# Kernel tuning notes

Hardware: AMD Instinct MI355X
Metric: run time of the kernel (lower is better)

The kernel has to match this reference:

```python
import jax, jax.numpy as jnp
import numpy as np

MARGIN = 0.3
EPS = 1e-6  # torch.nn.functional.pairwise_distance eps


def setup_inputs() -> dict:
    key = jax.random.key(0)
    k1, k2 = jax.random.split(key)
    B, D, C = 8192, 256, 512
    embeddings = jax.random.normal(k1, (B, D), dtype=jnp.float32)
    labels = jax.random.randint(k2, (B,), 0, C, dtype=jnp.int64)
    return {"embeddings": embeddings, "labels": labels}


def reference(embeddings, labels):
    B = embeddings.shape[0]
    # pairwise squared L2 via GEMM
    dot = embeddings @ embeddings.T                      # [B, B]
    sq = jnp.diag(dot)[:, None] + jnp.diag(dot)[None, :] - 2.0 * dot
    dist_sq = jnp.clip(sq, 0.0)

    same = labels[:, None] == labels[None, :]            # [B, B] bool
    eye = jnp.eye(B, dtype=bool)
    pos_mask = same & ~eye
    neg_mask = ~same

    valid = pos_mask.any(axis=1) & neg_mask.any(axis=1)  # [B]
    INF = dist_sq.max() + 1.0

    hardest_pos_idx = jnp.argmax(dist_sq * pos_mask.astype(dist_sq.dtype), axis=1)
    hardest_neg_idx = jnp.argmin(dist_sq + same.astype(dist_sq.dtype) * INF, axis=1)

    a = embeddings
    p = embeddings[hardest_pos_idx]
    n = embeddings[hardest_neg_idx]
    # torch pairwise_distance: ||x1 - x2 + eps||_2
    d_ap = jnp.linalg.norm(a - p + EPS, axis=1)
    d_an = jnp.linalg.norm(a - n + EPS, axis=1)
    per_anchor = jnp.maximum(d_ap - d_an + MARGIN, 0.0)

    v = valid.astype(per_anchor.dtype)
    n_valid = v.sum()
    loss = jnp.where(n_valid > 0, (per_anchor * v).sum() / jnp.maximum(n_valid, 1.0), 0.0)
    return loss
```

## Files before the change

kernel.cpp:

```cpp
#include <hip/hip_runtime.h>
#include <math.h>

#define NB 8192
#define ND 256
#define MARGIN_F 0.3f
#define EPS_F 1e-6f
#define BIAS_F 512.0f
#define NFIN 2048

typedef __attribute__((ext_vector_type(8))) short bf16x8;
typedef __attribute__((ext_vector_type(4))) float f32x4;

__device__ __forceinline__ unsigned short f2bf(float x) {
    unsigned int u = __float_as_uint(x);
    return (unsigned short)((u + 0x7fffu + ((u >> 16) & 1u)) >> 16);
}

__device__ __forceinline__ void gld16(const void* g, void* l) {
    __builtin_amdgcn_global_load_lds(
        (const __attribute__((address_space(1))) void*)g,
        (__attribute__((address_space(3))) void*)l, 16, 0, 0);
}

__global__ __launch_bounds__(512) void prep_k(const float* __restrict__ emb,
                                              unsigned short* __restrict__ ehi,
                                              float* __restrict__ sqnb,
                                              unsigned int* __restrict__ pos_key,
                                              unsigned int* __restrict__ neg_key) {
    const int tid = threadIdx.x;
    const int bid = blockIdx.x;
    const size_t base = (size_t)bid * 4096;

    const float4 v0 = *reinterpret_cast<const float4*>(&emb[base + tid * 8]);
    const float4 v1 = *reinterpret_cast<const float4*>(&emb[base + tid * 8 + 4]);
    ushort4 h0, h1;
    h0.x = f2bf(v0.x); h0.y = f2bf(v0.y); h0.z = f2bf(v0.z); h0.w = f2bf(v0.w);
    h1.x = f2bf(v1.x); h1.y = f2bf(v1.y); h1.z = f2bf(v1.z); h1.w = f2bf(v1.w);

    const int row_l = tid >> 5;
    const int kk = tid & 31;
    const int dst = (kk >> 2) * 512 + ((kk & 3) * 16 + row_l) * 8;
    *reinterpret_cast<ushort4*>(&ehi[base + dst])     = h0;
    *reinterpret_cast<ushort4*>(&ehi[base + dst + 4]) = h1;

    if (tid >= 64 && tid < 80)  pos_key[bid * 16 + (tid - 64)] = 0u;
    if (tid >= 80 && tid < 96)  neg_key[bid * 16 + (tid - 80)] = 0xFFFFFFFFu;

    float s = v0.x * v0.x + v0.y * v0.y + v0.z * v0.z + v0.w * v0.w
            + v1.x * v1.x + v1.y * v1.y + v1.z * v1.z + v1.w * v1.w;
#pragma unroll
    for (int m = 1; m <= 16; m <<= 1) s += __shfl_xor(s, m, 64);
    if (kk == 0) sqnb[bid * 16 + row_l] = s + BIAS_F;
}

template <bool DIAG>
__device__ __forceinline__ void mine_tile(
        const f32x4 (&acc)[2][4], const float (&sqjc)[4], const int (&lblc)[4],
        const unsigned (&enc)[4], const int* __restrict__ lbl_i_s,
        unsigned (&pmax)[8], unsigned (&nmin)[8],
        int i_base, int jb, int wrow, int q, int lx) {
#pragma unroll
    for (int tr = 0; tr < 2; ++tr) {
#pragma unroll
        for (int reg = 0; reg < 4; ++reg) {
            const int r = tr * 4 + reg;
            const int rowb = wrow + tr * 16 + q * 4 + reg;
            const int lab = lbl_i_s[rowb];
            unsigned pk[4], nk[4];
#pragma unroll
            for (int tc = 0; tc < 4; ++tc) {
                const float v = fmaf(-2.0f, acc[tr][tc][reg], sqjc[tc]);
                const unsigned key = (__float_as_uint(v) & 0xFFFFE000u) | enc[tc];
                const bool same = (lblc[tc] == lab);
                bool pc = same;
                if (DIAG) pc = same && ((jb + tc * 16 + lx) != (i_base + rowb));
                pk[tc] = pc ? key : 0u;
                nk[tc] = same ? 0xFFFFFFFFu : key;
            }
            const unsigned pa = pk[0] >= pk[1] ? pk[0] : pk[1];
            const unsigned pb = pk[2] >= pk[3] ? pk[2] : pk[3];
            const unsigned pm = pa >= pb ? pa : pb;
            pmax[r] = pmax[r] >= pm ? pmax[r] : pm;
            const unsigned na = nk[0] <= nk[1] ? nk[0] : nk[1];
            const unsigned nb = nk[2] <= nk[3] ? nk[2] : nk[3];
            const unsigned nm = na <= nb ? na : nb;
            nmin[r] = nmin[r] <= nm ? nmin[r] : nm;
        }
    }
}

__global__ __launch_bounds__(256, 4) void pair_k(
        const unsigned short* __restrict__ ehi, const float* __restrict__ sqnb,
        const int* __restrict__ labels,
        unsigned int* __restrict__ pos_key, unsigned int* __restrict__ neg_key) {
    __shared__ short Bsh[32 * 512];
    __shared__ int   lbl_i_s[128];

    const int tid = threadIdx.x;
    const int w = tid >> 6;
    const int lane = tid & 63;
    const int q = lane >> 4;
    const int lx = lane & 15;
    const int bid = blockIdx.x;
    const int slice = bid & 15;
    const int i_base = (bid >> 4) * 128;
    const int wrow = w * 32;
    const int g0 = (i_base >> 4) + w * 2;

    if (tid < 128) lbl_i_s[tid] = labels[i_base + tid];

    unsigned pmax[8], nmin[8];
#pragma unroll
    for (int r = 0; r < 8; ++r) { pmax[r] = 0u; nmin[r] = 0xFFFFFFFFu; }

#pragma unroll 1
    for (int jt = 0; jt < 8; ++jt) {
        const int jb = slice * 512 + jt * 64;
        __syncthreads();
        {
            const unsigned short* srcB = ehi + (size_t)(jb >> 4) * 4096;
#pragma unroll
            for (int p = 0; p < 8; ++p)
                gld16(srcB + ((size_t)p * 256 + tid) * 8, Bsh + (p * 256 + tid) * 8);
        }
        int lblc[4]; float sqjc[4]; unsigned enc[4];
#pragma unroll
        for (int tc = 0; tc < 4; ++tc) {
            const int jj = jb + tc * 16 + lx;
            lblc[tc] = labels[jj];
            sqjc[tc] = sqnb[jj];
            enc[tc] = 8191u - (unsigned)jj;
        }
        bf16x8 a0[2], a1[2], n0[2], n1[2];
#pragma unroll
        for (int tr = 0; tr < 2; ++tr) {
            a0[tr] = *(const bf16x8*)&ehi[((size_t)(g0 + tr) * 8 + 0) * 512 + lane * 8];
            a1[tr] = *(const bf16x8*)&ehi[((size_t)(g0 + tr) * 8 + 1) * 512 + lane * 8];
        }
        __syncthreads();

        f32x4 acc[2][4];
#pragma unroll
        for (int a = 0; a < 2; ++a)
#pragma unroll
            for (int b = 0; b < 4; ++b) acc[a][b] = (f32x4){0.f, 0.f, 0.f, 0.f};

#pragma unroll 1
        for (int kb2 = 0; kb2 < 4; ++kb2) {
            const int kbe = kb2 * 2, kbo = kbe + 1;
            const int kn0 = (kbe + 2) & 7, kn1 = (kbe + 3) & 7;
#pragma unroll
            for (int tr = 0; tr < 2; ++tr) {
                n0[tr] = *(const bf16x8*)&ehi[((size_t)(g0 + tr) * 8 + kn0) * 512 + lane * 8];
                n1[tr] = *(const bf16x8*)&ehi[((size_t)(g0 + tr) * 8 + kn1) * 512 + lane * 8];
            }
            {
                bf16x8 bh[4];
#pragma unroll
                for (int tc = 0; tc < 4; ++tc)
                    bh[tc] = *(const bf16x8*)&Bsh[(tc * 8 + kbe) * 512 + lane * 8];
#pragma unroll
                for (int tr = 0; tr < 2; ++tr)
#pragma unroll
                    for (int tc = 0; tc < 4; ++tc)
                        acc[tr][tc] = __builtin_amdgcn_mfma_f32_16x16x32_bf16(
                            a0[tr], bh[tc], acc[tr][tc], 0, 0, 0);
            }
            {
                bf16x8 bh[4];
#pragma unroll
                for (int tc = 0; tc < 4; ++tc)
                    bh[tc] = *(const bf16x8*)&Bsh[(tc * 8 + kbo) * 512 + lane * 8];
#pragma unroll
                for (int tr = 0; tr < 2; ++tr)
#pragma unroll
                    for (int tc = 0; tc < 4; ++tc)
                        acc[tr][tc] = __builtin_amdgcn_mfma_f32_16x16x32_bf16(
                            a1[tr], bh[tc], acc[tr][tc], 0, 0, 0);
            }
#pragma unroll
            for (int tr = 0; tr < 2; ++tr) { a0[tr] = n0[tr]; a1[tr] = n1[tr]; }
        }

        if ((unsigned)(jb - i_base) < 128u)
            mine_tile<true>(acc, sqjc, lblc, enc, lbl_i_s, pmax, nmin, i_base, jb, wrow, q, lx);
        else
            mine_tile<false>(acc, sqjc, lblc, enc, lbl_i_s, pmax, nmin, i_base, jb, wrow, q, lx);
    }

#pragma unroll
    for (int r = 0; r < 8; ++r) {
        unsigned pm = pmax[r], nm = nmin[r];
#pragma unroll
        for (int mm = 1; mm < 16; mm <<= 1) {
            const unsigned pm2 = __shfl_xor(pm, mm, 64);
            const unsigned nm2 = __shfl_xor(nm, mm, 64);
            pm = pm >= pm2 ? pm : pm2;
            nm = nm <= nm2 ? nm : nm2;
        }
        if (lx == r) {
            const int row = i_base + wrow + (r >> 2) * 16 + q * 4 + (r & 3);
            atomicMax(&pos_key[row], pm);
            atomicMin(&neg_key[row], nm);
        }
    }
}

__global__ __launch_bounds__(256) void final_k(
        const float* __restrict__ emb,
        const unsigned int* __restrict__ pos_key, const unsigned int* __restrict__ neg_key,
        float* __restrict__ pbsum, float* __restrict__ pbcnt) {
    __shared__ float ssum[4], scnt[4];
    const int w = threadIdx.x >> 6;
    const int lane = threadIdx.x & 63;
    const int i = blockIdx.x * 4 + w;

    const unsigned pk = pos_key[i], nk = neg_key[i];
    const int pi = 8191 - (int)(pk & 8191u);
    const int ni = 8191 - (int)(nk & 8191u);
    const bool valid = (pk != 0u) && (nk != 0xFFFFFFFFu);

    const float4 av  = *reinterpret_cast<const float4*>(&emb[(size_t)i  * ND + lane * 4]);
    const float4 pvv = *reinterpret_cast<const float4*>(&emb[(size_t)pi * ND + lane * 4]);
    const float4 nvv = *reinterpret_cast<const float4*>(&emb[(size_t)ni * ND + lane * 4]);
    float sap, san;
    {
        const float d0 = av.x - pvv.x + EPS_F, d1 = av.y - pvv.y + EPS_F;
        const float d2 = av.z - pvv.z + EPS_F, d3 = av.w - pvv.w + EPS_F;
        sap = d0 * d0 + d1 * d1 + d2 * d2 + d3 * d3;
        const float e0 = av.x - nvv.x + EPS_F, e1 = av.y - nvv.y + EPS_F;
        const float e2 = av.z - nvv.z + EPS_F, e3 = av.w - nvv.w + EPS_F;
        san = e0 * e0 + e1 * e1 + e2 * e2 + e3 * e3;
    }
#pragma unroll
    for (int m = 32; m; m >>= 1) {
        sap += __shfl_down(sap, m, 64);
        san += __shfl_down(san, m, 64);
    }
    if (lane == 0) {
        const float per = fmaxf(sqrtf(sap) - sqrtf(san) + MARGIN_F, 0.0f);
        ssum[w] = valid ? per : 0.0f;
        scnt[w] = valid ? 1.0f : 0.0f;
    }
    __syncthreads();
    if (threadIdx.x == 0) {
        pbsum[blockIdx.x] = ssum[0] + ssum[1] + ssum[2] + ssum[3];
        pbcnt[blockIdx.x] = scnt[0] + scnt[1] + scnt[2] + scnt[3];
    }
}

__global__ __launch_bounds__(256) void reduce_k(const float* __restrict__ pbsum,
                                                const float* __restrict__ pbcnt,
                                                float* __restrict__ out) {
    __shared__ float fs[4], fc[4];
    const int tid = threadIdx.x;
    float s = 0.0f, c = 0.0f;
#pragma unroll
    for (int r = 0; r < NFIN / 256; ++r) {
        s += pbsum[r * 256 + tid];
        c += pbcnt[r * 256 + tid];
    }
#pragma unroll
    for (int m = 32; m; m >>= 1) { s += __shfl_down(s, m, 64); c += __shfl_down(c, m, 64); }
    const int wv = tid >> 6, lane = tid & 63;
    if (lane == 0) { fs[wv] = s; fc[wv] = c; }
    __syncthreads();
    if (tid == 0) {
        const float S = fs[0] + fs[1] + fs[2] + fs[3];
        const float C = fc[0] + fc[1] + fc[2] + fc[3];
        out[0] = (C > 0.0f) ? (S / fmaxf(C, 1.0f)) : 0.0f;
    }
}

extern "C" void kernel_launch(void* const* d_in, const int* in_sizes, int n_in,
                              void* d_out, int out_size, void* d_ws, size_t ws_size,
                              hipStream_t stream) {
    const float* emb = (const float*)d_in[0];
    const int* labels = (const int*)d_in[1];
    float* out = (float*)d_out;

    char* ws = (char*)d_ws;
    unsigned short* ehi = (unsigned short*)ws;
    float* sqnb = (float*)(ws + (size_t)NB * ND * 2);
    unsigned int* pos_key = (unsigned int*)(sqnb + NB);
    unsigned int* neg_key = pos_key + NB;
    float* pbsum = (float*)(neg_key + NB);
    float* pbcnt = pbsum + NFIN;

    hipLaunchKernelGGL(prep_k, dim3(NB / 16), dim3(512), 0, stream,
                       emb, ehi, sqnb, pos_key, neg_key);
    hipLaunchKernelGGL(pair_k, dim3(1024), dim3(256), 0, stream,
                       ehi, sqnb, labels, pos_key, neg_key);
    hipLaunchKernelGGL(final_k, dim3(NFIN), dim3(256), 0, stream,
                       emb, pos_key, neg_key, pbsum, pbcnt);
    hipLaunchKernelGGL(reduce_k, dim3(1), dim3(256), 0, stream, pbsum, pbcnt, out);
}
```

Measured before the change: 118.1 us.

## Split B tile into K-halves and prefetch next tile's first half during compute

Splits the shared-memory B tile into two K halves, with the first half of each next j-tile prefetched asynchronously while the second half is still being multiplied. The A fragments are now loaded four k-blocks at a time instead of through the rolling register prefetch. The aim is to hide global-to-LDS load latency behind the MFMA work instead of stalling at a barrier on each tile. It adds an extra barrier per iteration and uses more registers for A fragments, which may lower occupancy.

```diff
diff --git a/kernel.cpp b/kernel.cpp
--- a/kernel.cpp
+++ b/kernel.cpp
@@ -93,7 +93,7 @@
         const unsigned short* __restrict__ ehi, const float* __restrict__ sqnb,
         const int* __restrict__ labels,
         unsigned int* __restrict__ pos_key, unsigned int* __restrict__ neg_key) {
-    __shared__ short Bsh[32 * 512];
+    __shared__ short Bsh[2 * 8192];
     __shared__ int   lbl_i_s[128];
 
     const int tid = threadIdx.x;
@@ -113,16 +113,26 @@
 #pragma unroll
     for (int r = 0; r < 8; ++r) { pmax[r] = 0u; nmin[r] = 0xFFFFFFFFu; }
 
+    {
+        const int jb0 = slice * 512;
+        const size_t gb = (size_t)(jb0 >> 4) * 4096 + tid * 8;
+#pragma unroll
+        for (int p = 0; p < 4; ++p)
+            gld16(ehi + gb + (size_t)p * 4096, Bsh + p * 2048 + tid * 8);
+    }
+    __syncthreads();
+
 #pragma unroll 1
     for (int jt = 0; jt < 8; ++jt) {
         const int jb = slice * 512 + jt * 64;
-        __syncthreads();
+
         {
-            const unsigned short* srcB = ehi + (size_t)(jb >> 4) * 4096;
-#pragma unroll
-            for (int p = 0; p < 8; ++p)
-                gld16(srcB + ((size_t)p * 256 + tid) * 8, Bsh + (p * 256 + tid) * 8);
-        }
+            const size_t gb = (size_t)(jb >> 4) * 4096 + 2048 + tid * 8;
+#pragma unroll
+            for (int p = 0; p < 4; ++p)
+                gld16(ehi + gb + (size_t)p * 4096, Bsh + 8192 + p * 2048 + tid * 8);
+        }
+
         int lblc[4]; float sqjc[4]; unsigned enc[4];
 #pragma unroll
         for (int tc = 0; tc < 4; ++tc) {
@@ -131,13 +141,6 @@
             sqjc[tc] = sqnb[jj];
             enc[tc] = 8191u - (unsigned)jj;
         }
-        bf16x8 a0[2], a1[2], n0[2], n1[2];
-#pragma unroll
-        for (int tr = 0; tr < 2; ++tr) {
-            a0[tr] = *(const bf16x8*)&ehi[((size_t)(g0 + tr) * 8 + 0) * 512 + lane * 8];
-            a1[tr] = *(const bf16x8*)&ehi[((size_t)(g0 + tr) * 8 + 1) * 512 + lane * 8];
-        }
-        __syncthreads();
 
         f32x4 acc[2][4];
 #pragma unroll
@@ -145,47 +148,66 @@
 #pragma unroll
             for (int b = 0; b < 4; ++b) acc[a][b] = (f32x4){0.f, 0.f, 0.f, 0.f};
 
-#pragma unroll 1
-        for (int kb2 = 0; kb2 < 4; ++kb2) {
-            const int kbe = kb2 * 2, kbo = kbe + 1;
-            const int kn0 = (kbe + 2) & 7, kn1 = (kbe + 3) & 7;
-#pragma unroll
-            for (int tr = 0; tr < 2; ++tr) {
-                n0[tr] = *(const bf16x8*)&ehi[((size_t)(g0 + tr) * 8 + kn0) * 512 + lane * 8];
-                n1[tr] = *(const bf16x8*)&ehi[((size_t)(g0 + tr) * 8 + kn1) * 512 + lane * 8];
-            }
-            {
+        {
+            bf16x8 af[4][2];
+#pragma unroll
+            for (int kbl = 0; kbl < 4; ++kbl)
+#pragma unroll
+                for (int tr = 0; tr < 2; ++tr)
+                    af[kbl][tr] = *(const bf16x8*)&ehi[
+                        ((size_t)(g0 + tr) * 8 + kbl) * 512 + lane * 8];
+#pragma unroll
+            for (int kbl = 0; kbl < 4; ++kbl) {
                 bf16x8 bh[4];
 #pragma unroll
                 for (int tc = 0; tc < 4; ++tc)
-                    bh[tc] = *(const bf16x8*)&Bsh[(tc * 8 + kbe) * 512 + lane * 8];
+                    bh[tc] = *(const bf16x8*)&Bsh[tc * 2048 + kbl * 512 + lane * 8];
 #pragma unroll
                 for (int tr = 0; tr < 2; ++tr)
 #pragma unroll
                     for (int tc = 0; tc < 4; ++tc)
                         acc[tr][tc] = __builtin_amdgcn_mfma_f32_16x16x32_bf16(
-                            a0[tr], bh[tc], acc[tr][tc], 0, 0, 0);
+                            af[kbl][tr], bh[tc], acc[tr][tc], 0, 0, 0);
             }
-            {
+        }
+        __syncthreads();
+
+        if (jt < 7) {
+            const size_t gb = (size_t)((jb + 64) >> 4) * 4096 + tid * 8;
+#pragma unroll
+            for (int p = 0; p < 4; ++p)
+                gld16(ehi + gb + (size_t)p * 4096, Bsh + p * 2048 + tid * 8);
+        }
+
+        {
+            bf16x8 af[4][2];
+#pragma unroll
+            for (int kbl = 0; kbl < 4; ++kbl)
+#pragma unroll
+                for (int tr = 0; tr < 2; ++tr)
+                    af[kbl][tr] = *(const bf16x8*)&ehi[
+                        ((size_t)(g0 + tr) * 8 + 4 + kbl) * 512 + lane * 8];
+#pragma unroll
+            for (int kbl = 0; kbl < 4; ++kbl) {
                 bf16x8 bh[4];
 #pragma unroll
                 for (int tc = 0; tc < 4; ++tc)
-                    bh[tc] = *(const bf16x8*)&Bsh[(tc * 8 + kbo) * 512 + lane * 8];
+                    bh[tc] = *(const bf16x8*)&Bsh[8192 + tc * 2048 + kbl * 512 + lane * 8];
 #pragma unroll
                 for (int tr = 0; tr < 2; ++tr)
 #pragma unroll
                     for (int tc = 0; tc < 4; ++tc)
                         acc[tr][tc] = __builtin_amdgcn_mfma_f32_16x16x32_bf16(
-                            a1[tr], bh[tc], acc[tr][tc], 0, 0, 0);
+                            af[kbl][tr], bh[tc], acc[tr][tc], 0, 0, 0);
             }
-#pragma unroll
-            for (int tr = 0; tr < 2; ++tr) { a0[tr] = n0[tr]; a1[tr] = n1[tr]; }
         }
 
         if ((unsigned)(jb - i_base) < 128u)
             mine_tile<true>(acc, sqjc, lblc, enc, lbl_i_s, pmax, nmin, i_base, jb, wrow, q, lx);
         else
             mine_tile<false>(acc, sqjc, lblc, enc, lbl_i_s, pmax, nmin, i_base, jb, wrow, q, lx);
+
+        __syncthreads();
     }
 
 #pragma unroll
```

Measured after the change: 135.7 us. 1.15x slower.
